# Performance work log

Hardware: AMD Instinct MI355X
Metric: run time of the kernel (lower is better)

Reference implementation:

```python
import jax, jax.numpy as jnp
import numpy as np

DIM = 64; HEADS = 8; WIN = 4; K = 3
B = 8; H = 256; W = 256; WS = H // 2  # 2x2 window grid since ka_win_num=4
L = WIN * K * K            # 36 tokens for kernel self-attention
DH = DIM // HEADS
RED = DIM // 16            # SE reduction (dim>=64 branch)


def setup_inputs() -> dict:
    key = jax.random.key(0)
    ks = jax.random.split(key, 12)
    f = lambda k, s: jax.random.normal(k, s, jnp.float32) * 0.05
    return {
        "x": jax.random.normal(ks[0], (B, DIM, H, W), jnp.float32),
        "conv_w": f(ks[1], (WIN, DIM, DIM, K, K)),   # per-window Conv2d weights
        "w_qkv": f(ks[2], (3 * DIM, DIM)),
        "b_qkv": f(ks[3], (3 * DIM,)),
        "w_out": f(ks[4], (DIM, DIM)),
        "b_out": f(ks[5], (DIM,)),
        "se_w1": f(ks[6], (WIN, RED, DIM)),
        "se_b1": f(ks[7], (WIN, RED)),
        "se_w2": f(ks[8], (WIN, DIM, RED)),
        "se_b2": f(ks[9], (WIN, DIM)),
        "ln_w": jnp.ones((DIM,), jnp.float32),
        "ln_b": jnp.zeros((DIM,), jnp.float32),
    }


def reference(x, conv_w, w_qkv, b_qkv, w_out, b_out,
              se_w1, se_b1, se_w2, se_b2, ln_w, ln_b):
    Bx, C, Hx, Wx = x.shape
    ws = WS
    xw = x.reshape(Bx, C, 2, ws, 2, ws).transpose(2, 4, 0, 1, 3, 5)
    xw = xw.reshape(WIN, Bx, C, ws, ws)

    # ---- kernels from conv weights (conv output itself is discarded upstream)
    kern = conv_w.reshape(WIN, DIM, DIM, K * K).transpose(1, 0, 3, 2).reshape(DIM, L, DIM)

    # ---- tiny multi-head self-attention over the L kernel tokens, batch = DIM
    qkv = kern @ w_qkv.T + b_qkv                       # (DIM, L, 3*DIM)
    qkv = qkv.reshape(DIM, L, 3, HEADS, DH).transpose(2, 0, 3, 1, 4)  # (3, DIM, H, L, DH)
    q = qkv[0] * (DH ** -0.5)
    k_, v = qkv[1], qkv[2]
    attn = jax.nn.softmax(jnp.einsum('bhld,bhmd->bhlm', q, k_), axis=-1)
    out = jnp.einsum('bhlm,bhmd->bhld', attn, v)        # (DIM, H, L, DH)
    out = out.transpose(0, 2, 1, 3).reshape(DIM, L, DIM)
    kern = out @ w_out.T + b_out                        # (DIM, L, DIM)
    kern = kern.reshape(DIM, WIN, K, K, DIM).transpose(1, 0, 4, 2, 3)

    # ---- SE gating per window: pool over spatial, two 1x1 convs, sigmoid gate
    pooled = kern.mean(axis=(3, 4))
    h = jax.nn.relu(jnp.einsum('woi,wri->wor', pooled, se_w1) + se_b1[:, None, :])
    s = jax.nn.sigmoid(jnp.einsum('wor,wir->woi', h, se_w2) + se_b2[:, None, :])
    kern = kern * s[:, :, :, None, None]

    # ---- dynamic per-window conv2d (stride 1, pad 1)
    conv = lambda xi, wi: jax.lax.conv_general_dilated(
        xi, wi, window_strides=(1, 1), padding=((1, 1), (1, 1)))
    yw = jax.vmap(conv)(xw, kern)

    # ---- window reverse -> (B, C, H, W)
    y = yw.reshape(2, 2, Bx, C, ws, ws).transpose(2, 3, 0, 4, 1, 5).reshape(Bx, C, Hx, Wx)

    # ---- channel-last LayerNorm, then residual
    yt = y.transpose(0, 2, 3, 1)
    mu = yt.mean(-1, keepdims=True)
    var = yt.var(-1, keepdims=True)
    yt = (yt - mu) / jnp.sqrt(var + 1e-5) * ln_w + ln_b
    return x + yt.transpose(0, 3, 1, 2)
```

## Files before the change

kernel.cpp:

```cpp
#include <hip/hip_runtime.h>
#include <hip/hip_fp16.h>


typedef __attribute__((ext_vector_type(8))) _Float16 half8;
typedef __attribute__((ext_vector_type(4))) float floatx4;
typedef unsigned short ushort_t;

__device__ __forceinline__ ushort_t f2h(float f) {
  union { _Float16 h; ushort_t u; } cv;
  cv.h = (_Float16)f;
  return cv.u;
}

__device__ __align__(16) ushort_t g_W2[4 * 9 * 64 * 64];

__global__ __launch_bounds__(256) void tw_kernel(
    const float* __restrict__ conv_w,
    const float* __restrict__ w_qkv,
    const float* __restrict__ b_qkv,
    const float* __restrict__ w_out,
    const float* __restrict__ b_out,
    const float* __restrict__ se_w1,
    const float* __restrict__ se_b1,
    const float* __restrict__ se_w2,
    const float* __restrict__ se_b2)
{
  __shared__ __align__(16) float smem[11952];
  const int t = threadIdx.x;
  const int o = blockIdx.x;
  float* k0   = smem;
  float* qkvb = smem + 2448;
  float* aout = smem + 9504;

  for (int idx = t; idx < 36 * 64; idx += 256) {
    int l = idx >> 6, i = idx & 63;
    int win = l / 9, t9 = l - win * 9;
    k0[l * 68 + i] = conv_w[((win * 64 + o) * 64 + i) * 9 + t9];
  }
  __syncthreads();

  for (int idx = t; idx < 48 * 36; idx += 256) {
    int jg = idx / 36, l = idx - jg * 36;
    int j = jg << 2;
    const float* kr = k0 + l * 68;
    const float* w0 = w_qkv + j * 64;
    float a0 = 0.f, a1 = 0.f, a2 = 0.f, a3 = 0.f;
    #pragma unroll
    for (int i = 0; i < 64; i += 4) {
      floatx4 kf  = *(const floatx4*)(kr + i);
      floatx4 wf0 = *(const floatx4*)(w0 + i);
      floatx4 wf1 = *(const floatx4*)(w0 + 64 + i);
      floatx4 wf2 = *(const floatx4*)(w0 + 128 + i);
      floatx4 wf3 = *(const floatx4*)(w0 + 192 + i);
      #pragma unroll
      for (int e = 0; e < 4; ++e) {
        a0 += kf[e] * wf0[e];
        a1 += kf[e] * wf1[e];
        a2 += kf[e] * wf2[e];
        a3 += kf[e] * wf3[e];
      }
    }
    floatx4 r = { a0 + b_qkv[j],     a1 + b_qkv[j + 1],
                  a2 + b_qkv[j + 2], a3 + b_qkv[j + 3] };
    *(floatx4*)(qkvb + l * 196 + j) = r;
  }
  __syncthreads();

  for (int idx = t; idx < 288; idx += 256) {
    int h = idx / 36, l = idx - h * 36;
    const int hq = h << 3;
    floatx4 q0 = *(const floatx4*)(qkvb + l * 196 + hq);
    floatx4 q1 = *(const floatx4*)(qkvb + l * 196 + hq + 4);
    float sc[36];
    float mx = -1e30f;
    #pragma unroll
    for (int m = 0; m < 36; ++m) {
      const float* kr = qkvb + m * 196 + 64 + hq;
      floatx4 k0f = *(const floatx4*)(kr);
      floatx4 k1f = *(const floatx4*)(kr + 4);
      float s = 0.f;
      #pragma unroll
      for (int e = 0; e < 4; ++e) s += q0[e] * k0f[e];
      #pragma unroll
      for (int e = 0; e < 4; ++e) s += q1[e] * k1f[e];
      s *= 0.35355339059327373f;
      sc[m] = s;
      mx = fmaxf(mx, s);
    }
    float den = 0.f;
    #pragma unroll
    for (int m = 0; m < 36; ++m) { sc[m] = __expf(sc[m] - mx); den += sc[m]; }
    float a[8];
    #pragma unroll
    for (int e = 0; e < 8; ++e) a[e] = 0.f;
    #pragma unroll
    for (int m = 0; m < 36; ++m) {
      const float* vr = qkvb + m * 196 + 128 + hq;
      floatx4 v0f = *(const floatx4*)(vr);
      floatx4 v1f = *(const floatx4*)(vr + 4);
      float p = sc[m];
      #pragma unroll
      for (int e = 0; e < 4; ++e) { a[e] += p * v0f[e]; a[e + 4] += p * v1f[e]; }
    }
    float inv = 1.f / den;
    floatx4 o0, o1;
    #pragma unroll
    for (int e = 0; e < 4; ++e) { o0[e] = a[e] * inv; o1[e] = a[e + 4] * inv; }
    *(floatx4*)(aout + l * 68 + hq) = o0;
    *(floatx4*)(aout + l * 68 + hq + 4) = o1;
  }
  __syncthreads();

  float* mat = k0;
  for (int idx = t; idx < 16 * 36; idx += 256) {
    int og = idx / 36, l = idx - og * 36;
    int oo = og << 2;
    const float* ar = aout + l * 68;
    const float* w0 = w_out + oo * 64;
    float a0 = 0.f, a1 = 0.f, a2 = 0.f, a3 = 0.f;
    #pragma unroll
    for (int i = 0; i < 64; i += 4) {
      floatx4 af  = *(const floatx4*)(ar + i);
      floatx4 wf0 = *(const floatx4*)(w0 + i);
      floatx4 wf1 = *(const floatx4*)(w0 + 64 + i);
      floatx4 wf2 = *(const floatx4*)(w0 + 128 + i);
      floatx4 wf3 = *(const floatx4*)(w0 + 192 + i);
      #pragma unroll
      for (int e = 0; e < 4; ++e) {
        a0 += af[e] * wf0[e];
        a1 += af[e] * wf1[e];
        a2 += af[e] * wf2[e];
        a3 += af[e] * wf3[e];
      }
    }
    floatx4 r = { a0 + b_out[oo],     a1 + b_out[oo + 1],
                  a2 + b_out[oo + 2], a3 + b_out[oo + 3] };
    *(floatx4*)(mat + l * 68 + oo) = r;
  }
  __syncthreads();

  float* pl = qkvb;
  float* h1 = qkvb + 256;
  {
    int win = t >> 6, I = t & 63;
    float p = 0.f;
    #pragma unroll
    for (int t9 = 0; t9 < 9; ++t9) p += mat[(win * 9 + t9) * 68 + I];
    pl[t] = p * (1.f / 9.f);
  }
  __syncthreads();
  if (t < 16) {
    int win = t >> 2, r = t & 3;
    const float* wr = se_w1 + (win * 4 + r) * 64;
    const float* pr = pl + (win << 6);
    float a = se_b1[win * 4 + r];
    #pragma unroll 8
    for (int i = 0; i < 64; ++i) a += pr[i] * wr[i];
    h1[t] = fmaxf(a, 0.f);
  }
  __syncthreads();
  {
    int win = t >> 6, I = t & 63;
    float a = se_b2[(win << 6) + I];
    #pragma unroll
    for (int r = 0; r < 4; ++r)
      a += h1[win * 4 + r] * se_w2[((win << 6) + I) * 4 + r];
    float s = 1.f / (1.f + __expf(-a));
    #pragma unroll
    for (int t9 = 0; t9 < 9; ++t9) {
      float v = mat[(win * 9 + t9) * 68 + I] * s;
      g_W2[((win * 9 + t9) * 64 + o) * 64 + I] = f2h(v);
    }
  }
}

__global__ __launch_bounds__(256, 5) void conv_kernel(
    const float* __restrict__ x,
    const float* __restrict__ ln_w,
    const float* __restrict__ ln_b,
    float* __restrict__ outp)
{
  __shared__ __align__(16) short xs[14688];
  int* xs32 = (int*)xs;
  const int t = threadIdx.x;
  const int wb = blockIdx.x & 7;
  const int hb = (blockIdx.x >> 3) & 63;
  const int b  = blockIdx.x >> 9;
  const int gh0 = hb << 2, gw0 = wb << 5;
  const int hlo = (gh0 >= 128) ? 128 : 0;
  const int wlo = (gw0 >= 128) ? 128 : 0;
  const int win = ((gh0 >= 128) ? 2 : 0) + ((gw0 >= 128) ? 1 : 0);
  const float* xb = x + ((size_t)b << 22);

  #pragma unroll
  for (int it = 0; it < 3; ++it) {
    int idx = t + it * 256;
    int u = idx & 3;
    int r = (idx >> 2) % 6;
    int cp = idx / 24;
    int gh = gh0 + r - 1;
    int gw = gw0 + (u << 3);
    floatx4 a0 = {0.f, 0.f, 0.f, 0.f}, a1 = a0, b0 = a0, b1 = a0;
    if (gh >= hlo && gh < hlo + 128) {
      const float* p = xb + ((size_t)(2 * cp) << 16) + gh * 256 + gw;
      a0 = *(const floatx4*)p;
      a1 = *(const floatx4*)(p + 4);
      b0 = *(const floatx4*)(p + 65536);
      b1 = *(const floatx4*)(p + 65540);
    }
    int base = (r * 34 + (u << 3) + 1) * 36 + cp;
    #pragma unroll
    for (int j = 0; j < 4; ++j) {
      unsigned int pv = (unsigned int)f2h(a0[j]) |
                        ((unsigned int)f2h(b0[j]) << 16);
      xs32[base + j * 36] = (int)pv;
    }
    #pragma unroll
    for (int j = 0; j < 4; ++j) {
      unsigned int pv = (unsigned int)f2h(a1[j]) |
                        ((unsigned int)f2h(b1[j]) << 16);
      xs32[base + (j + 4) * 36] = (int)pv;
    }
  }
  #pragma unroll
  for (int it = 0; it < 2; ++it) {
    int idx = t + it * 256;
    if (idx < 384) {
      int e = idx & 1;
      int r = (idx >> 1) % 6;
      int cp = idx / 12;
      int gh = gh0 + r - 1;
      int gw = e ? (gw0 + 32) : (gw0 - 1);
      int cl = e ? 33 : 0;
      unsigned int pv = 0;
      if (gh >= hlo && gh < hlo + 128 && gw >= wlo && gw < wlo + 128) {
        const float* p = xb + ((size_t)(2 * cp) << 16) + gh * 256 + gw;
        pv = (unsigned int)f2h(p[0]) | ((unsigned int)f2h(p[65536]) << 16);
      }
      xs32[(r * 34 + cl) * 36 + cp] = (int)pv;
    }
  }
  __syncthreads();

  const int wave = t >> 6, lane = t & 63;
  const int l15 = lane & 15, q = lane >> 4;

  floatx4 acc[2][4];
  #pragma unroll
  for (int mt = 0; mt < 2; ++mt)
    #pragma unroll
    for (int nt = 0; nt < 4; ++nt)
      acc[mt][nt] = (floatx4){0.f, 0.f, 0.f, 0.f};

  int aoff[2];
  #pragma unroll
  for (int mt = 0; mt < 2; ++mt)
    aoff[mt] = (wave * 34 + (mt << 4) + l15) * 72 + (q << 3);

  const ushort_t* Wb = g_W2 + win * 36864 + l15 * 64 + (q << 3);
  half8 bcur[4], bnxt[4];
  #pragma unroll
  for (int nt = 0; nt < 4; ++nt)
    bcur[nt] = *(const half8*)(Wb + nt * 1024);

  #pragma unroll
  for (int tap = 0; tap < 9; ++tap) {
    const int ky = tap / 3, kx = tap - ky * 3;
    const int toff = (ky * 34 + kx) * 72;
    #pragma unroll
    for (int kc = 0; kc < 2; ++kc) {
      const int nit = tap * 2 + kc + 1;
      if (nit < 18) {
        const int ntap = nit >> 1, nkc = nit & 1;
        #pragma unroll
        for (int nt = 0; nt < 4; ++nt)
          bnxt[nt] = *(const half8*)(Wb + ntap * 4096 + nkc * 32 + nt * 1024);
      }
      half8 av[2];
      #pragma unroll
      for (int mt = 0; mt < 2; ++mt)
        av[mt] = *(const half8*)(xs + aoff[mt] + toff + kc * 32);
      #pragma unroll
      for (int mt = 0; mt < 2; ++mt)
        #pragma unroll
        for (int nt = 0; nt < 4; ++nt)
          acc[mt][nt] = __builtin_amdgcn_mfma_f32_16x16x32_f16(
              av[mt], bcur[nt], acc[mt][nt], 0, 0, 0);
      #pragma unroll
      for (int nt = 0; nt < 4; ++nt) bcur[nt] = bnxt[nt];
    }
  }

  float lnwv[4], lnbv[4];
  #pragma unroll
  for (int nt = 0; nt < 4; ++nt) {
    int c = (nt << 4) + l15;
    lnwv[nt] = ln_w[c];
    lnbv[nt] = ln_b[c];
  }
  #pragma unroll
  for (int mt = 0; mt < 2; ++mt) {
    const int colb = mt << 4;
    floatx4 xr[4];
    size_t goffs[4];
    #pragma unroll
    for (int nt = 0; nt < 4; ++nt) {
      const int c = (nt << 4) + l15;
      goffs[nt] = ((size_t)(b * 64 + c) << 16) +
                  (gh0 + wave) * 256 + gw0 + colb + (q << 2);
      xr[nt] = *(const floatx4*)(x + goffs[nt]);
    }
    float s1[4], s2[4];
    #pragma unroll
    for (int e = 0; e < 4; ++e) { s1[e] = 0.f; s2[e] = 0.f; }
    #pragma unroll
    for (int nt = 0; nt < 4; ++nt)
      #pragma unroll
      for (int e = 0; e < 4; ++e) {
        float v = acc[mt][nt][e];
        s1[e] += v;
        s2[e] += v * v;
      }
    #pragma unroll
    for (int m = 1; m < 16; m <<= 1) {
      #pragma unroll
      for (int e = 0; e < 4; ++e) {
        s1[e] += __shfl_xor(s1[e], m, 64);
        s2[e] += __shfl_xor(s2[e], m, 64);
      }
    }
    float mean[4], rstd[4];
    #pragma unroll
    for (int e = 0; e < 4; ++e) {
      mean[e] = s1[e] * 0.015625f;
      float var = s2[e] * 0.015625f - mean[e] * mean[e];
      rstd[e] = rsqrtf(var + 1e-5f);
    }
    #pragma unroll
    for (int nt = 0; nt < 4; ++nt) {
      floatx4 v;
      #pragma unroll
      for (int e = 0; e < 4; ++e)
        v[e] = (acc[mt][nt][e] - mean[e]) * rstd[e] * lnwv[nt] + lnbv[nt] + xr[nt][e];
      *(floatx4*)(outp + goffs[nt]) = v;
    }
  }
}

extern "C" void kernel_launch(void* const* d_in, const int* in_sizes, int n_in,
                              void* d_out, int out_size, void* d_ws, size_t ws_size,
                              hipStream_t stream) {
  const float* x     = (const float*)d_in[0];
  const float* convw = (const float*)d_in[1];
  const float* wqkv  = (const float*)d_in[2];
  const float* bqkv  = (const float*)d_in[3];
  const float* wout  = (const float*)d_in[4];
  const float* bout  = (const float*)d_in[5];
  const float* sew1  = (const float*)d_in[6];
  const float* seb1  = (const float*)d_in[7];
  const float* sew2  = (const float*)d_in[8];
  const float* seb2  = (const float*)d_in[9];
  const float* lnw   = (const float*)d_in[10];
  const float* lnb   = (const float*)d_in[11];
  float* outp = (float*)d_out;

  hipLaunchKernelGGL(tw_kernel, dim3(64), dim3(256), 0, stream,
                     convw, wqkv, bqkv, wout, bout,
                     sew1, seb1, sew2, seb2);
  hipLaunchKernelGGL(conv_kernel, dim3(4096), dim3(256), 0, stream,
                     x, lnw, lnb, outp);
}
```

Measured before the change: 465.7 us.

## Make conv kernel persistent over batch with register-prefetched input tiles

Each conv block now loops over all 8 batch images for one spatial tile instead of handling a single (batch, tile) pair, so the grid shrinks from 4096 to 512 blocks. The next image's input tile is prefetched into registers while the current image runs its MFMA loop and LayerNorm epilogue, then written to LDS between barriers. This aims to hide global load latency and to reuse the per-window weights in cache across the batch loop. In exchange occupancy drops (launch bounds 5 to 2, with more live registers), and 512 blocks may underfill the GPU's CUs.

```diff
diff --git a/kernel.cpp b/kernel.cpp
--- a/kernel.cpp
+++ b/kernel.cpp
@@ -174,7 +174,7 @@
   }
 }
 
-__global__ __launch_bounds__(256, 5) void conv_kernel(
+__global__ __launch_bounds__(256, 2) void conv_kernel(
     const float* __restrict__ x,
     const float* __restrict__ ln_w,
     const float* __restrict__ ln_b,
@@ -184,73 +184,92 @@
   int* xs32 = (int*)xs;
   const int t = threadIdx.x;
   const int wb = blockIdx.x & 7;
-  const int hb = (blockIdx.x >> 3) & 63;
-  const int b  = blockIdx.x >> 9;
+  const int hb = blockIdx.x >> 3;
   const int gh0 = hb << 2, gw0 = wb << 5;
   const int hlo = (gh0 >= 128) ? 128 : 0;
   const int wlo = (gw0 >= 128) ? 128 : 0;
   const int win = ((gh0 >= 128) ? 2 : 0) + ((gw0 >= 128) ? 1 : 0);
-  const float* xb = x + ((size_t)b << 22);
-
-  #pragma unroll
-  for (int it = 0; it < 3; ++it) {
-    int idx = t + it * 256;
-    int u = idx & 3;
-    int r = (idx >> 2) % 6;
-    int cp = idx / 24;
-    int gh = gh0 + r - 1;
-    int gw = gw0 + (u << 3);
-    floatx4 a0 = {0.f, 0.f, 0.f, 0.f}, a1 = a0, b0 = a0, b1 = a0;
-    if (gh >= hlo && gh < hlo + 128) {
-      const float* p = xb + ((size_t)(2 * cp) << 16) + gh * 256 + gw;
-      a0 = *(const floatx4*)p;
-      a1 = *(const floatx4*)(p + 4);
-      b0 = *(const floatx4*)(p + 65536);
-      b1 = *(const floatx4*)(p + 65540);
-    }
-    int base = (r * 34 + (u << 3) + 1) * 36 + cp;
-    #pragma unroll
-    for (int j = 0; j < 4; ++j) {
-      unsigned int pv = (unsigned int)f2h(a0[j]) |
-                        ((unsigned int)f2h(b0[j]) << 16);
-      xs32[base + j * 36] = (int)pv;
-    }
-    #pragma unroll
-    for (int j = 0; j < 4; ++j) {
-      unsigned int pv = (unsigned int)f2h(a1[j]) |
-                        ((unsigned int)f2h(b1[j]) << 16);
-      xs32[base + (j + 4) * 36] = (int)pv;
-    }
-  }
-  #pragma unroll
-  for (int it = 0; it < 2; ++it) {
-    int idx = t + it * 256;
-    if (idx < 384) {
-      int e = idx & 1;
-      int r = (idx >> 1) % 6;
-      int cp = idx / 12;
+
+  floatx4 sa0[3], sa1[3], sb0[3], sb1[3];
+  float se0[2], se1[2];
+
+  auto load_regs = [&](int bb) {
+    const float* xb = x + ((size_t)bb << 22);
+    #pragma unroll
+    for (int it = 0; it < 3; ++it) {
+      int idx = t + it * 256;
+      int u = idx & 3;
+      int r = (idx >> 2) % 6;
+      int cp = idx / 24;
       int gh = gh0 + r - 1;
-      int gw = e ? (gw0 + 32) : (gw0 - 1);
-      int cl = e ? 33 : 0;
-      unsigned int pv = 0;
-      if (gh >= hlo && gh < hlo + 128 && gw >= wlo && gw < wlo + 128) {
+      int gw = gw0 + (u << 3);
+      floatx4 z = {0.f, 0.f, 0.f, 0.f};
+      sa0[it] = z; sa1[it] = z; sb0[it] = z; sb1[it] = z;
+      if (gh >= hlo && gh < hlo + 128) {
         const float* p = xb + ((size_t)(2 * cp) << 16) + gh * 256 + gw;
-        pv = (unsigned int)f2h(p[0]) | ((unsigned int)f2h(p[65536]) << 16);
-      }
-      xs32[(r * 34 + cl) * 36 + cp] = (int)pv;
-    }
-  }
-  __syncthreads();
+        sa0[it] = *(const floatx4*)p;
+        sa1[it] = *(const floatx4*)(p + 4);
+        sb0[it] = *(const floatx4*)(p + 65536);
+        sb1[it] = *(const floatx4*)(p + 65540);
+      }
+    }
+    #pragma unroll
+    for (int it = 0; it < 2; ++it) {
+      int idx = t + it * 256;
+      se0[it] = 0.f; se1[it] = 0.f;
+      if (idx < 384) {
+        int e = idx & 1;
+        int r = (idx >> 1) % 6;
+        int cp = idx / 12;
+        int gh = gh0 + r - 1;
+        int gw = e ? (gw0 + 32) : (gw0 - 1);
+        if (gh >= hlo && gh < hlo + 128 && gw >= wlo && gw < wlo + 128) {
+          const float* p = xb + ((size_t)(2 * cp) << 16) + gh * 256 + gw;
+          se0[it] = p[0];
+          se1[it] = p[65536];
+        }
+      }
+    }
+  };
+
+  auto write_lds = [&]() {
+    #pragma unroll
+    for (int it = 0; it < 3; ++it) {
+      int idx = t + it * 256;
+      int u = idx & 3;
+      int r = (idx >> 2) % 6;
+      int cp = idx / 24;
+      int base = (r * 34 + (u << 3) + 1) * 36 + cp;
+      #pragma unroll
+      for (int j = 0; j < 4; ++j) {
+        unsigned int pv = (unsigned int)f2h(sa0[it][j]) |
+                          ((unsigned int)f2h(sb0[it][j]) << 16);
+        xs32[base + j * 36] = (int)pv;
+      }
+      #pragma unroll
+      for (int j = 0; j < 4; ++j) {
+        unsigned int pv = (unsigned int)f2h(sa1[it][j]) |
+                          ((unsigned int)f2h(sb1[it][j]) << 16);
+        xs32[base + (j + 4) * 36] = (int)pv;
+      }
+    }
+    #pragma unroll
+    for (int it = 0; it < 2; ++it) {
+      int idx = t + it * 256;
+      if (idx < 384) {
+        int e = idx & 1;
+        int r = (idx >> 1) % 6;
+        int cp = idx / 12;
+        int cl = e ? 33 : 0;
+        unsigned int pv = (unsigned int)f2h(se0[it]) |
+                          ((unsigned int)f2h(se1[it]) << 16);
+        xs32[(r * 34 + cl) * 36 + cp] = (int)pv;
+      }
+    }
+  };
 
   const int wave = t >> 6, lane = t & 63;
   const int l15 = lane & 15, q = lane >> 4;
-
-  floatx4 acc[2][4];
-  #pragma unroll
-  for (int mt = 0; mt < 2; ++mt)
-    #pragma unroll
-    for (int nt = 0; nt < 4; ++nt)
-      acc[mt][nt] = (floatx4){0.f, 0.f, 0.f, 0.f};
 
   int aoff[2];
   #pragma unroll
@@ -258,38 +277,6 @@
     aoff[mt] = (wave * 34 + (mt << 4) + l15) * 72 + (q << 3);
 
   const ushort_t* Wb = g_W2 + win * 36864 + l15 * 64 + (q << 3);
-  half8 bcur[4], bnxt[4];
-  #pragma unroll
-  for (int nt = 0; nt < 4; ++nt)
-    bcur[nt] = *(const half8*)(Wb + nt * 1024);
-
-  #pragma unroll
-  for (int tap = 0; tap < 9; ++tap) {
-    const int ky = tap / 3, kx = tap - ky * 3;
-    const int toff = (ky * 34 + kx) * 72;
-    #pragma unroll
-    for (int kc = 0; kc < 2; ++kc) {
-      const int nit = tap * 2 + kc + 1;
-      if (nit < 18) {
-        const int ntap = nit >> 1, nkc = nit & 1;
-        #pragma unroll
-        for (int nt = 0; nt < 4; ++nt)
-          bnxt[nt] = *(const half8*)(Wb + ntap * 4096 + nkc * 32 + nt * 1024);
-      }
-      half8 av[2];
-      #pragma unroll
-      for (int mt = 0; mt < 2; ++mt)
-        av[mt] = *(const half8*)(xs + aoff[mt] + toff + kc * 32);
-      #pragma unroll
-      for (int mt = 0; mt < 2; ++mt)
-        #pragma unroll
-        for (int nt = 0; nt < 4; ++nt)
-          acc[mt][nt] = __builtin_amdgcn_mfma_f32_16x16x32_f16(
-              av[mt], bcur[nt], acc[mt][nt], 0, 0, 0);
-      #pragma unroll
-      for (int nt = 0; nt < 4; ++nt) bcur[nt] = bnxt[nt];
-    }
-  }
 
   float lnwv[4], lnbv[4];
   #pragma unroll
@@ -298,51 +285,107 @@
     lnwv[nt] = ln_w[c];
     lnbv[nt] = ln_b[c];
   }
-  #pragma unroll
-  for (int mt = 0; mt < 2; ++mt) {
-    const int colb = mt << 4;
-    floatx4 xr[4];
-    size_t goffs[4];
-    #pragma unroll
-    for (int nt = 0; nt < 4; ++nt) {
-      const int c = (nt << 4) + l15;
-      goffs[nt] = ((size_t)(b * 64 + c) << 16) +
-                  (gh0 + wave) * 256 + gw0 + colb + (q << 2);
-      xr[nt] = *(const floatx4*)(x + goffs[nt]);
-    }
-    float s1[4], s2[4];
-    #pragma unroll
-    for (int e = 0; e < 4; ++e) { s1[e] = 0.f; s2[e] = 0.f; }
+
+  load_regs(0);
+  write_lds();
+  load_regs(1);
+  __syncthreads();
+
+  #pragma unroll 1
+  for (int b = 0; b < 8; ++b) {
+    floatx4 acc[2][4];
+    #pragma unroll
+    for (int mt = 0; mt < 2; ++mt)
+      #pragma unroll
+      for (int nt = 0; nt < 4; ++nt)
+        acc[mt][nt] = (floatx4){0.f, 0.f, 0.f, 0.f};
+
+    half8 bcur[4], bnxt[4];
     #pragma unroll
     for (int nt = 0; nt < 4; ++nt)
+      bcur[nt] = *(const half8*)(Wb + nt * 1024);
+
+    #pragma unroll
+    for (int tap = 0; tap < 9; ++tap) {
+      const int ky = tap / 3, kx = tap - ky * 3;
+      const int toff = (ky * 34 + kx) * 72;
+      #pragma unroll
+      for (int kc = 0; kc < 2; ++kc) {
+        const int nit = tap * 2 + kc + 1;
+        if (nit < 18) {
+          const int ntap = nit >> 1, nkc = nit & 1;
+          #pragma unroll
+          for (int nt = 0; nt < 4; ++nt)
+            bnxt[nt] = *(const half8*)(Wb + ntap * 4096 + nkc * 32 + nt * 1024);
+        }
+        half8 av[2];
+        #pragma unroll
+        for (int mt = 0; mt < 2; ++mt)
+          av[mt] = *(const half8*)(xs + aoff[mt] + toff + kc * 32);
+        #pragma unroll
+        for (int mt = 0; mt < 2; ++mt)
+          #pragma unroll
+          for (int nt = 0; nt < 4; ++nt)
+            acc[mt][nt] = __builtin_amdgcn_mfma_f32_16x16x32_f16(
+                av[mt], bcur[nt], acc[mt][nt], 0, 0, 0);
+        #pragma unroll
+        for (int nt = 0; nt < 4; ++nt) bcur[nt] = bnxt[nt];
+      }
+    }
+
+    #pragma unroll
+    for (int mt = 0; mt < 2; ++mt) {
+      const int colb = mt << 4;
+      floatx4 xr[4];
+      size_t goffs[4];
+      #pragma unroll
+      for (int nt = 0; nt < 4; ++nt) {
+        const int c = (nt << 4) + l15;
+        goffs[nt] = ((size_t)(b * 64 + c) << 16) +
+                    (gh0 + wave) * 256 + gw0 + colb + (q << 2);
+        xr[nt] = *(const floatx4*)(x + goffs[nt]);
+      }
+      float s1[4], s2[4];
+      #pragma unroll
+      for (int e = 0; e < 4; ++e) { s1[e] = 0.f; s2[e] = 0.f; }
+      #pragma unroll
+      for (int nt = 0; nt < 4; ++nt)
+        #pragma unroll
+        for (int e = 0; e < 4; ++e) {
+          float v = acc[mt][nt][e];
+          s1[e] += v;
+          s2[e] += v * v;
+        }
+      #pragma unroll
+      for (int m = 1; m < 16; m <<= 1) {
+        #pragma unroll
+        for (int e = 0; e < 4; ++e) {
+          s1[e] += __shfl_xor(s1[e], m, 64);
+          s2[e] += __shfl_xor(s2[e], m, 64);
+        }
+      }
+      float mean[4], rstd[4];
       #pragma unroll
       for (int e = 0; e < 4; ++e) {
-        float v = acc[mt][nt][e];
-        s1[e] += v;
-        s2[e] += v * v;
-      }
-    #pragma unroll
-    for (int m = 1; m < 16; m <<= 1) {
-      #pragma unroll
-      for (int e = 0; e < 4; ++e) {
-        s1[e] += __shfl_xor(s1[e], m, 64);
-        s2[e] += __shfl_xor(s2[e], m, 64);
-      }
-    }
-    float mean[4], rstd[4];
-    #pragma unroll
-    for (int e = 0; e < 4; ++e) {
-      mean[e] = s1[e] * 0.015625f;
-      float var = s2[e] * 0.015625f - mean[e] * mean[e];
-      rstd[e] = rsqrtf(var + 1e-5f);
-    }
-    #pragma unroll
-    for (int nt = 0; nt < 4; ++nt) {
-      floatx4 v;
-      #pragma unroll
-      for (int e = 0; e < 4; ++e)
-        v[e] = (acc[mt][nt][e] - mean[e]) * rstd[e] * lnwv[nt] + lnbv[nt] + xr[nt][e];
-      *(floatx4*)(outp + goffs[nt]) = v;
+        mean[e] = s1[e] * 0.015625f;
+        float var = s2[e] * 0.015625f - mean[e] * mean[e];
+        rstd[e] = rsqrtf(var + 1e-5f);
+      }
+      #pragma unroll
+      for (int nt = 0; nt < 4; ++nt) {
+        floatx4 v;
+        #pragma unroll
+        for (int e = 0; e < 4; ++e)
+          v[e] = (acc[mt][nt][e] - mean[e]) * rstd[e] * lnwv[nt] + lnbv[nt] + xr[nt][e];
+        *(floatx4*)(outp + goffs[nt]) = v;
+      }
+    }
+
+    if (b < 7) {
+      __syncthreads();
+      write_lds();
+      if (b < 6) load_regs(b + 2);
+      __syncthreads();
     }
   }
 }
@@ -367,6 +410,6 @@
   hipLaunchKernelGGL(tw_kernel, dim3(64), dim3(256), 0, stream,
                      convw, wqkv, bqkv, wout, bout,
                      sew1, seb1, sew2, seb2);
-  hipLaunchKernelGGL(conv_kernel, dim3(4096), dim3(256), 0, stream,
+  hipLaunchKernelGGL(conv_kernel, dim3(512), dim3(256), 0, stream,
                      x, lnw, lnb, outp);
 }
```

New measurement: 500.7 us. 7.5% more time.
